# Kernel optimization log

Measured on AMD Instinct MI355X. Metric: run time of the kernel, lower is better.

## Reference

```python
import jax, jax.numpy as jnp
import numpy as np

B, N, L, K, C1 = 128, 300, 600, 19, 100  # batch, num_cnns, input_length, filter_size, fc hidden
PS = 7  # pool size == stride
LC = L - (K - 1)               # 582, conv output length
LP = (LC - PS) // PS + 1       # 83, pooled length
NC = 2                         # num_classes
EPS = 1e-5


def _bn(x, g, b, m, v):
    # eval-mode batchnorm, params broadcast along given axes already
    return g * (x - m) * jax.lax.rsqrt(v + EPS) + b


def setup_inputs() -> dict:
    key = jax.random.key(0)
    ks = jax.random.split(key, 20)
    f = lambda i, shape, s=0.1: (jax.random.normal(ks[i], shape, dtype=jnp.float32) * s)
    pv = lambda i, shape: (jax.random.uniform(ks[i], shape, dtype=jnp.float32) + 0.5)
    return {
        'x': jax.random.normal(ks[0], (B, 4, L), dtype=jnp.float32),
        'conv_w': f(1, (N, 4, K)), 'conv_b': f(2, (N,)),
        'bn1_g': pv(3, (N,)), 'bn1_b': f(4, (N,)), 'bn1_m': f(5, (N,)), 'bn1_v': pv(6, (N,)),
        'fc1_w': f(7, (N, C1, LP)), 'fc1_b': f(8, (N, C1)),
        'bn2_g': pv(9, (N, C1)), 'bn2_b': f(10, (N, C1)), 'bn2_m': f(11, (N, C1)), 'bn2_v': pv(12, (N, C1)),
        'fc2_w': f(13, (N, C1)), 'fc2_b': f(14, (N,)),
        'bn3_g': pv(15, (N,)), 'bn3_b': f(16, (N,)), 'bn3_m': f(17, (N,)), 'bn3_v': pv(18, (N,)),
        'final_w': f(19, (NC, N)), 'final_b': jnp.zeros((NC,), dtype=jnp.float32),
    }


def reference(x, conv_w, conv_b, bn1_g, bn1_b, bn1_m, bn1_v,
              fc1_w, fc1_b, bn2_g, bn2_b, bn2_m, bn2_v,
              fc2_w, fc2_b, bn3_g, bn3_b, bn3_m, bn3_v,
              final_w, final_b):
    # grouped conv on a repeated input == plain conv with 4 in-channels, N out-channels
    h = jax.lax.conv_general_dilated(x, conv_w, window_strides=(1,), padding='VALID',
                                     dimension_numbers=('NCH', 'OIH', 'NCH'))  # [B,N,582]
    h = h + conv_b[None, :, None]
    h = _bn(h, bn1_g[None, :, None], bn1_b[None, :, None], bn1_m[None, :, None], bn1_v[None, :, None])
    h = jnp.exp(h)
    # MaxPool1d(7,7): [B,N,582] -> [B,N,83]
    h = jax.lax.reduce_window(h, -jnp.inf, jax.lax.max,
                              window_dimensions=(1, 1, PS), window_strides=(1, 1, PS), padding='VALID')
    # grouped 1x1 conv == per-unit dense: [B,N,83] x [N,100,83] -> [B,N,100]
    h = jnp.einsum('bnp,nhp->bnh', h, fc1_w) + fc1_b[None]
    h = jax.nn.relu(_bn(h, bn2_g[None], bn2_b[None], bn2_m[None], bn2_v[None]))
    # second grouped 1x1 conv: [B,N,100] x [N,100] -> [B,N]
    h = jnp.einsum('bnh,nh->bn', h, fc2_w) + fc2_b[None]
    h = jax.nn.relu(_bn(h, bn3_g[None], bn3_b[None], bn3_m[None], bn3_v[None]))
    return h @ final_w.T + final_b  # [B,num_classes]
```

## Files before the change

### kernel.cpp

```cpp
#include <hip/hip_runtime.h>
#include <math.h>

#define EPS_ 1e-5f

__global__ __launch_bounds__(256) void kP(const float* __restrict__ conv_w,
                                          float* __restrict__ cw4) {
    const int cq = blockIdx.x;
    const int c  = cq / 5;
    const int kq = cq - c * 5;
    for (int n = threadIdx.x; n < 300; n += 256) {
        float4 v;
        const int k0 = 4 * kq;
        v.x = (k0 + 0 < 19) ? conv_w[n * 76 + c * 19 + k0 + 0] : 0.f;
        v.y = (k0 + 1 < 19) ? conv_w[n * 76 + c * 19 + k0 + 1] : 0.f;
        v.z = (k0 + 2 < 19) ? conv_w[n * 76 + c * 19 + k0 + 2] : 0.f;
        v.w = (k0 + 3 < 19) ? conv_w[n * 76 + c * 19 + k0 + 3] : 0.f;
        reinterpret_cast<float4*>(cw4)[(c * 5 + kq) * 300 + n] = v;
    }
}

__global__ __launch_bounds__(64) void kA(
        const float* __restrict__ x,
        const float* __restrict__ cw4,
        const float* __restrict__ conv_b,
        const float* __restrict__ g1, const float* __restrict__ b1,
        const float* __restrict__ m1, const float* __restrict__ v1,
        float* __restrict__ pooled)
{
    const int id  = blockIdx.x;
    const int b   = id / 112;
    const int sub = id - b * 112;
    if (sub >= 105) return;
    const int ng  = sub / 21;
    const int pc  = sub - ng * 21;
    const int p0c = pc * 4;
    const int p0  = (p0c > 79) ? 79 : p0c;
    const int lane = threadIdx.x;
    const int n   = ng * 64 + lane;
    const int nc  = (n < 300) ? n : 299;

    const float4* w4 = reinterpret_cast<const float4*>(cw4);

    float acc[28];
    #pragma unroll
    for (int i = 0; i < 28; ++i) acc[i] = 0.f;

    #pragma unroll 1
    for (int c = 0; c < 4; ++c) {
        const float* xc = x + b * 2400 + c * 600 + 7 * p0;
        float xw[46];
        #pragma unroll
        for (int j = 0; j < 46; ++j) xw[j] = xc[j];
        #pragma unroll
        for (int kq = 0; kq < 5; ++kq) {
            const float4 wv = w4[(c * 5 + kq) * 300 + nc];
            const int ni = (kq == 4) ? 3 : 4;
            #pragma unroll
            for (int i = 0; i < ni; ++i) {
                const int k = 4 * kq + i;
                const float wvv = (i == 0) ? wv.x : (i == 1) ? wv.y
                                : (i == 2) ? wv.z : wv.w;
                #pragma unroll
                for (int p = 0; p < 4; ++p)
                    #pragma unroll
                    for (int q = 0; q < 7; ++q)
                        acc[p * 7 + q] = fmaf(xw[7 * p + q + k], wvv,
                                              acc[p * 7 + q]);
            }
        }
    }

    const float A1 = g1[nc] * rsqrtf(v1[nc] + EPS_);
    const float B1 = fmaf(A1, conv_b[nc] - m1[nc], b1[nc]);
    if (n < 300) {
        float* op = pooled + ((size_t)n * 83 + p0) * 128 + b;
        #pragma unroll
        for (int p = 0; p < 4; ++p) {
            float mx = -INFINITY;
            #pragma unroll
            for (int q = 0; q < 7; ++q)
                mx = fmaxf(mx, fmaf(A1, acc[p * 7 + q], B1));
            op[p * 128] = __expf(mx);
        }
    }
}

__global__ __launch_bounds__(256, 2) void kB(
        const float* __restrict__ pooled,
        const float* __restrict__ fc1w,
        const float* __restrict__ fc1b,
        const float* __restrict__ g2, const float* __restrict__ b2,
        const float* __restrict__ m2, const float* __restrict__ v2,
        const float* __restrict__ fc2w,
        const float* __restrict__ fc2b,
        const float* __restrict__ g3, const float* __restrict__ b3,
        const float* __restrict__ m3, const float* __restrict__ v3,
        float* __restrict__ sout)
{
    __shared__ __align__(16) float sW[83 * 116];
    __shared__ float sRed[4][64];
    const int id  = blockIdx.x;
    const int n   = id >> 1;
    const int bh  = id & 1;
    const int tid = threadIdx.x;

    {
        const float* src = fc1w + (size_t)n * 8300;
        for (int i = tid; i < 8300; i += 256) {
            const int h = i / 83, p = i - h * 83;
            sW[p * 116 + h] = src[i];
        }
        for (int i = tid; i < 83 * 16; i += 256) {
            const int p = i / 16, h = 100 + (i - p * 16);
            sW[p * 116 + h] = 0.f;
        }
    }
    __syncthreads();

    const int lane = tid & 63;
    const int wv   = __builtin_amdgcn_readfirstlane(tid >> 6);
    const int h0   = wv * 28;
    const int bb   = bh * 64 + lane;

    const float* pp = pooled + (size_t)n * 83 * 128 + bb;

    float acc[28];
    #pragma unroll
    for (int j = 0; j < 28; ++j) acc[j] = 0.f;

    #pragma unroll 4
    for (int p = 0; p < 83; ++p) {
        const float pv = pp[p * 128];
        const float* wrow = sW + p * 116 + h0;
        #pragma unroll
        for (int jq = 0; jq < 7; ++jq) {
            const float4 w = *reinterpret_cast<const float4*>(wrow + 4 * jq);
            acc[jq * 4 + 0] = fmaf(w.x, pv, acc[jq * 4 + 0]);
            acc[jq * 4 + 1] = fmaf(w.y, pv, acc[jq * 4 + 1]);
            acc[jq * 4 + 2] = fmaf(w.z, pv, acc[jq * 4 + 2]);
            acc[jq * 4 + 3] = fmaf(w.w, pv, acc[jq * 4 + 3]);
        }
    }

    const int nh = (wv < 3) ? 28 : 16;
    float part = 0.f;
    for (int j = 0; j < nh; ++j) {
        const int hi = n * 100 + h0 + j;
        const float A2 = g2[hi] * rsqrtf(v2[hi] + EPS_);
        const float C2 = fmaf(A2, fc1b[hi] - m2[hi], b2[hi]);
        part = fmaf(fmaxf(fmaf(A2, acc[j], C2), 0.f), fc2w[hi], part);
    }
    sRed[wv][lane] = part;
    __syncthreads();

    if (tid < 64) {
        float s = sRed[0][tid] + sRed[1][tid] + sRed[2][tid] + sRed[3][tid];
        s += fc2b[n];
        const float A3 = g3[n] * rsqrtf(v3[n] + EPS_);
        const float z = fmaf(A3, s - m3[n], b3[n]);
        sout[n * 128 + bh * 64 + tid] = fmaxf(z, 0.f);
    }
}

__global__ __launch_bounds__(64) void kC(
        const float* __restrict__ sout,
        const float* __restrict__ fw,
        const float* __restrict__ fb,
        float* __restrict__ out)
{
    const int b = blockIdx.x, t = threadIdx.x;
    float a0 = 0.f, a1 = 0.f;
    for (int nn = t; nn < 300; nn += 64) {
        const float v = sout[nn * 128 + b];
        a0 = fmaf(v, fw[nn], a0);
        a1 = fmaf(v, fw[300 + nn], a1);
    }
    #pragma unroll
    for (int off = 32; off > 0; off >>= 1) {
        a0 += __shfl_xor(a0, off, 64);
        a1 += __shfl_xor(a1, off, 64);
    }
    if (t == 0) {
        out[b * 2 + 0] = a0 + fb[0];
        out[b * 2 + 1] = a1 + fb[1];
    }
}

extern "C" void kernel_launch(void* const* d_in, const int* in_sizes, int n_in,
                              void* d_out, int out_size, void* d_ws, size_t ws_size,
                              hipStream_t stream) {
    const float* x      = (const float*)d_in[0];
    const float* conv_w = (const float*)d_in[1];
    const float* conv_b = (const float*)d_in[2];
    const float* g1 = (const float*)d_in[3];
    const float* b1 = (const float*)d_in[4];
    const float* m1 = (const float*)d_in[5];
    const float* v1 = (const float*)d_in[6];
    const float* fc1_w = (const float*)d_in[7];
    const float* fc1_b = (const float*)d_in[8];
    const float* g2 = (const float*)d_in[9];
    const float* b2 = (const float*)d_in[10];
    const float* m2 = (const float*)d_in[11];
    const float* v2 = (const float*)d_in[12];
    const float* fc2_w = (const float*)d_in[13];
    const float* fc2_b = (const float*)d_in[14];
    const float* g3 = (const float*)d_in[15];
    const float* b3 = (const float*)d_in[16];
    const float* m3 = (const float*)d_in[17];
    const float* v3 = (const float*)d_in[18];
    const float* fw = (const float*)d_in[19];
    const float* fb = (const float*)d_in[20];
    float* out = (float*)d_out;

    float* pooled = (float*)d_ws;
    float* cw4    = pooled + (size_t)300 * 83 * 128;
    float* sout   = cw4 + 24000;

    kP<<<20, 256, 0, stream>>>(conv_w, cw4);
    kA<<<128 * 112, 64, 0, stream>>>(x, cw4, conv_b, g1, b1, m1, v1, pooled);
    kB<<<600, 256, 0, stream>>>(pooled, fc1_w, fc1_b, g2, b2, m2, v2,
                                fc2_w, fc2_b, g3, b3, m3, v3, sout);
    kC<<<128, 64, 0, stream>>>(sout, fw, fb, out);
}
```

Measured before the change: 174.3 us.

## Compute conv stage with fp16 MFMA matrix instructions instead of scalar FMAs

```diff
diff --git a/kernel.cpp b/kernel.cpp
--- a/kernel.cpp
+++ b/kernel.cpp
@@ -3,85 +3,114 @@
 
 #define EPS_ 1e-5f
 
-__global__ __launch_bounds__(256) void kP(const float* __restrict__ conv_w,
-                                          float* __restrict__ cw4) {
-    const int cq = blockIdx.x;
-    const int c  = cq / 5;
-    const int kq = cq - c * 5;
-    for (int n = threadIdx.x; n < 300; n += 256) {
-        float4 v;
-        const int k0 = 4 * kq;
-        v.x = (k0 + 0 < 19) ? conv_w[n * 76 + c * 19 + k0 + 0] : 0.f;
-        v.y = (k0 + 1 < 19) ? conv_w[n * 76 + c * 19 + k0 + 1] : 0.f;
-        v.z = (k0 + 2 < 19) ? conv_w[n * 76 + c * 19 + k0 + 2] : 0.f;
-        v.w = (k0 + 3 < 19) ? conv_w[n * 76 + c * 19 + k0 + 3] : 0.f;
-        reinterpret_cast<float4*>(cw4)[(c * 5 + kq) * 300 + n] = v;
-    }
-}
-
-__global__ __launch_bounds__(64) void kA(
+typedef _Float16 half8 __attribute__((ext_vector_type(8)));
+typedef float floatx4 __attribute__((ext_vector_type(4)));
+
+__global__ __launch_bounds__(256) void kW(const float* __restrict__ conv_w,
+                                          unsigned short* __restrict__ wT) {
+    const int idx = blockIdx.x * 256 + threadIdx.x;
+    if (idx >= 304 * 96) return;
+    const int n = idx / 96, k = idx - n * 96;
+    const int c = k / 24, kk = k - c * 24;
+    float v = (n < 300 && kk < 19) ? conv_w[n * 76 + c * 19 + kk] : 0.f;
+    union { _Float16 h; unsigned short u; } cv;
+    cv.h = (_Float16)v;
+    wT[idx] = cv.u;
+}
+
+__global__ __launch_bounds__(64) void kM(
         const float* __restrict__ x,
-        const float* __restrict__ cw4,
+        const unsigned short* __restrict__ wT,
         const float* __restrict__ conv_b,
         const float* __restrict__ g1, const float* __restrict__ b1,
         const float* __restrict__ m1, const float* __restrict__ v1,
         float* __restrict__ pooled)
 {
-    const int id  = blockIdx.x;
-    const int b   = id / 112;
-    const int sub = id - b * 112;
-    if (sub >= 105) return;
-    const int ng  = sub / 21;
-    const int pc  = sub - ng * 21;
-    const int p0c = pc * 4;
-    const int p0  = (p0c > 79) ? 79 : p0c;
+    const int id = blockIdx.x;
+    const int b  = id / 24;
+    const int nt = id - b * 24;
+    if (nt >= 19) return;
     const int lane = threadIdx.x;
-    const int n   = ng * 64 + lane;
-    const int nc  = (n < 300) ? n : 299;
-
-    const float4* w4 = reinterpret_cast<const float4*>(cw4);
-
-    float acc[28];
-    #pragma unroll
-    for (int i = 0; i < 28; ++i) acc[i] = 0.f;
-
-    #pragma unroll 1
-    for (int c = 0; c < 4; ++c) {
-        const float* xc = x + b * 2400 + c * 600 + 7 * p0;
-        float xw[46];
+    const int ln   = lane & 15;
+    const int quad = lane >> 4;
+    const int n0   = nt * 16;
+
+    __shared__ float xs[4 * 704];
+    __shared__ float dbuf[16 * 116];
+
+    for (int i = lane; i < 4 * 704; i += 64) {
+        const int c = i / 704, t = i - c * 704;
+        xs[i] = (t < 600) ? x[b * 2400 + c * 600 + t] : 0.f;
+    }
+
+    half8 bf[3];
+    {
+        const unsigned short* wrow = wT + (n0 + ln) * 96 + quad * 8;
         #pragma unroll
-        for (int j = 0; j < 46; ++j) xw[j] = xc[j];
-        #pragma unroll
-        for (int kq = 0; kq < 5; ++kq) {
-            const float4 wv = w4[(c * 5 + kq) * 300 + nc];
-            const int ni = (kq == 4) ? 3 : 4;
+        for (int s = 0; s < 3; ++s) {
+            union { int4 i; half8 h; } u;
+            u.i = *reinterpret_cast<const int4*>(wrow + 32 * s);
+            bf[s] = u.h;
+        }
+    }
+
+    int cS[3], oS[3];
+    #pragma unroll
+    for (int s = 0; s < 3; ++s) {
+        const int kg0 = 32 * s + 8 * quad;
+        cS[s] = kg0 / 24; oS[s] = kg0 - cS[s] * 24;
+    }
+
+    const int nq = lane & 3;
+    float A1w[4], B1w[4];
+    #pragma unroll
+    for (int w = 0; w < 4; ++w) {
+        const int n = n0 + 4 * nq + w;
+        const int nc = (n < 300) ? n : 299;
+        A1w[w] = g1[nc] * rsqrtf(v1[nc] + EPS_);
+        B1w[w] = fmaf(A1w[w], conv_b[nc] - m1[nc], b1[nc]);
+    }
+    __syncthreads();
+
+    for (int ci = 0; ci < 6; ++ci) {
+        const int t0 = 112 * ci;
+        #pragma unroll 1
+        for (int mt = 0; mt < 7; ++mt) {
+            const int tb = t0 + 16 * mt + ln;
+            floatx4 acc = {0.f, 0.f, 0.f, 0.f};
             #pragma unroll
-            for (int i = 0; i < ni; ++i) {
-                const int k = 4 * kq + i;
-                const float wvv = (i == 0) ? wv.x : (i == 1) ? wv.y
-                                : (i == 2) ? wv.z : wv.w;
+            for (int s = 0; s < 3; ++s) {
+                const float* px = &xs[cS[s] * 704 + tb + oS[s]];
+                half8 af;
                 #pragma unroll
-                for (int p = 0; p < 4; ++p)
+                for (int j = 0; j < 8; ++j)
+                    af[j] = (_Float16)px[j];
+                acc = __builtin_amdgcn_mfma_f32_16x16x32_f16(af, bf[s], acc,
+                                                             0, 0, 0);
+            }
+            float* dp = &dbuf[ln * 116 + 16 * mt + quad * 4];
+            float4 dv = make_float4(acc[0], acc[1], acc[2], acc[3]);
+            *reinterpret_cast<float4*>(dp) = dv;
+        }
+        __syncthreads();
+        const int pl = lane >> 2;
+        const int npool = (ci < 5) ? 16 : 3;
+        if (pl < npool) {
+            const int pg = 16 * ci + pl;
+            #pragma unroll
+            for (int w = 0; w < 4; ++w) {
+                const int n = n0 + 4 * nq + w;
+                if (n < 300) {
+                    const float* dq = &dbuf[(4 * nq + w) * 116 + 7 * pl];
+                    float mx = -INFINITY;
                     #pragma unroll
                     for (int q = 0; q < 7; ++q)
-                        acc[p * 7 + q] = fmaf(xw[7 * p + q + k], wvv,
-                                              acc[p * 7 + q]);
+                        mx = fmaxf(mx, fmaf(A1w[w], dq[q], B1w[w]));
+                    pooled[((size_t)n * 83 + pg) * 128 + b] = __expf(mx);
+                }
             }
         }
-    }
-
-    const float A1 = g1[nc] * rsqrtf(v1[nc] + EPS_);
-    const float B1 = fmaf(A1, conv_b[nc] - m1[nc], b1[nc]);
-    if (n < 300) {
-        float* op = pooled + ((size_t)n * 83 + p0) * 128 + b;
-        #pragma unroll
-        for (int p = 0; p < 4; ++p) {
-            float mx = -INFINITY;
-            #pragma unroll
-            for (int q = 0; q < 7; ++q)
-                mx = fmaxf(mx, fmaf(A1, acc[p * 7 + q], B1));
-            op[p * 128] = __expf(mx);
-        }
+        __syncthreads();
     }
 }
 
@@ -213,11 +242,11 @@
     float* out = (float*)d_out;
 
     float* pooled = (float*)d_ws;
-    float* cw4    = pooled + (size_t)300 * 83 * 128;
-    float* sout   = cw4 + 24000;
-
-    kP<<<20, 256, 0, stream>>>(conv_w, cw4);
-    kA<<<128 * 112, 64, 0, stream>>>(x, cw4, conv_b, g1, b1, m1, v1, pooled);
+    float* sout   = pooled + (size_t)300 * 83 * 128;
+    unsigned short* wT = (unsigned short*)(sout + 38400);
+
+    kW<<<114, 256, 0, stream>>>(conv_w, wT);
+    kM<<<128 * 24, 64, 0, stream>>>(x, wT, conv_b, g1, b1, m1, v1, pooled);
     kB<<<600, 256, 0, stream>>>(pooled, fc1_w, fc1_b, g2, b2, m2, v2,
                                 fc2_w, fc2_b, g3, b3, m3, v3, sout);
     kC<<<128, 64, 0, stream>>>(sout, fw, fb, out);
```

Result: slower. 186.9 us (+7.3%).

## Split fc1 hidden dimension across two blocks and defer bn3 to final kernel

Applied to the files above, without the earlier changes.

```diff
diff --git a/kernel.cpp b/kernel.cpp
--- a/kernel.cpp
+++ b/kernel.cpp
@@ -85,85 +85,80 @@
     }
 }
 
-__global__ __launch_bounds__(256, 2) void kB(
+__global__ __launch_bounds__(256) void kB(
         const float* __restrict__ pooled,
         const float* __restrict__ fc1w,
         const float* __restrict__ fc1b,
         const float* __restrict__ g2, const float* __restrict__ b2,
         const float* __restrict__ m2, const float* __restrict__ v2,
         const float* __restrict__ fc2w,
+        float* __restrict__ sp)
+{
+    __shared__ float sW[83 * 60];
+    __shared__ float sRed[4][64];
+    const int id  = blockIdx.x;
+    const int n   = id >> 2;
+    const int rem = id & 3;
+    const int bh  = rem >> 1;
+    const int hq  = rem & 1;
+    const int tid = threadIdx.x;
+
+    {
+        const float* src = fc1w + (size_t)n * 8300 + hq * 50 * 83;
+        for (int i = tid; i < 4150; i += 256) {
+            const int h = i / 83, p = i - h * 83;
+            sW[p * 60 + h] = src[i];
+        }
+        for (int i = tid; i < 830; i += 256) {
+            const int p = i / 10, h = 50 + (i - p * 10);
+            sW[p * 60 + h] = 0.f;
+        }
+    }
+    __syncthreads();
+
+    const int lane = tid & 63;
+    const int wv   = __builtin_amdgcn_readfirstlane(tid >> 6);
+    const int h0   = wv * 13;
+    const int nh   = (wv < 3) ? 13 : 11;
+    const int bb   = bh * 64 + lane;
+
+    const float* pp = pooled + (size_t)n * 83 * 128 + bb;
+
+    float acc[13];
+    #pragma unroll
+    for (int j = 0; j < 13; ++j) acc[j] = 0.f;
+
+    #pragma unroll 4
+    for (int p = 0; p < 83; ++p) {
+        const float pv = pp[p * 128];
+        const float* wrow = sW + p * 60 + h0;
+        #pragma unroll
+        for (int j = 0; j < 13; ++j)
+            acc[j] = fmaf(wrow[j], pv, acc[j]);
+    }
+
+    const int hbase = n * 100 + hq * 50 + h0;
+    float part = 0.f;
+    for (int j = 0; j < nh; ++j) {
+        const int hi = hbase + j;
+        const float A2 = g2[hi] * rsqrtf(v2[hi] + EPS_);
+        const float C2 = fmaf(A2, fc1b[hi] - m2[hi], b2[hi]);
+        part = fmaf(fmaxf(fmaf(A2, acc[j], C2), 0.f), fc2w[hi], part);
+    }
+    sRed[wv][lane] = part;
+    __syncthreads();
+
+    if (tid < 64) {
+        const float s = sRed[0][tid] + sRed[1][tid] + sRed[2][tid] + sRed[3][tid];
+        sp[((size_t)hq * 300 + n) * 128 + bh * 64 + tid] = s;
+    }
+}
+
+__global__ __launch_bounds__(64) void kC(
+        const float* __restrict__ sp,
         const float* __restrict__ fc2b,
         const float* __restrict__ g3, const float* __restrict__ b3,
         const float* __restrict__ m3, const float* __restrict__ v3,
-        float* __restrict__ sout)
-{
-    __shared__ __align__(16) float sW[83 * 116];
-    __shared__ float sRed[4][64];
-    const int id  = blockIdx.x;
-    const int n   = id >> 1;
-    const int bh  = id & 1;
-    const int tid = threadIdx.x;
-
-    {
-        const float* src = fc1w + (size_t)n * 8300;
-        for (int i = tid; i < 8300; i += 256) {
-            const int h = i / 83, p = i - h * 83;
-            sW[p * 116 + h] = src[i];
-        }
-        for (int i = tid; i < 83 * 16; i += 256) {
-            const int p = i / 16, h = 100 + (i - p * 16);
-            sW[p * 116 + h] = 0.f;
-        }
-    }
-    __syncthreads();
-
-    const int lane = tid & 63;
-    const int wv   = __builtin_amdgcn_readfirstlane(tid >> 6);
-    const int h0   = wv * 28;
-    const int bb   = bh * 64 + lane;
-
-    const float* pp = pooled + (size_t)n * 83 * 128 + bb;
-
-    float acc[28];
-    #pragma unroll
-    for (int j = 0; j < 28; ++j) acc[j] = 0.f;
-
-    #pragma unroll 4
-    for (int p = 0; p < 83; ++p) {
-        const float pv = pp[p * 128];
-        const float* wrow = sW + p * 116 + h0;
-        #pragma unroll
-        for (int jq = 0; jq < 7; ++jq) {
-            const float4 w = *reinterpret_cast<const float4*>(wrow + 4 * jq);
-            acc[jq * 4 + 0] = fmaf(w.x, pv, acc[jq * 4 + 0]);
-            acc[jq * 4 + 1] = fmaf(w.y, pv, acc[jq * 4 + 1]);
-            acc[jq * 4 + 2] = fmaf(w.z, pv, acc[jq * 4 + 2]);
-            acc[jq * 4 + 3] = fmaf(w.w, pv, acc[jq * 4 + 3]);
-        }
-    }
-
-    const int nh = (wv < 3) ? 28 : 16;
-    float part = 0.f;
-    for (int j = 0; j < nh; ++j) {
-        const int hi = n * 100 + h0 + j;
-        const float A2 = g2[hi] * rsqrtf(v2[hi] + EPS_);
-        const float C2 = fmaf(A2, fc1b[hi] - m2[hi], b2[hi]);
-        part = fmaf(fmaxf(fmaf(A2, acc[j], C2), 0.f), fc2w[hi], part);
-    }
-    sRed[wv][lane] = part;
-    __syncthreads();
-
-    if (tid < 64) {
-        float s = sRed[0][tid] + sRed[1][tid] + sRed[2][tid] + sRed[3][tid];
-        s += fc2b[n];
-        const float A3 = g3[n] * rsqrtf(v3[n] + EPS_);
-        const float z = fmaf(A3, s - m3[n], b3[n]);
-        sout[n * 128 + bh * 64 + tid] = fmaxf(z, 0.f);
-    }
-}
-
-__global__ __launch_bounds__(64) void kC(
-        const float* __restrict__ sout,
         const float* __restrict__ fw,
         const float* __restrict__ fb,
         float* __restrict__ out)
@@ -171,9 +166,11 @@
     const int b = blockIdx.x, t = threadIdx.x;
     float a0 = 0.f, a1 = 0.f;
     for (int nn = t; nn < 300; nn += 64) {
-        const float v = sout[nn * 128 + b];
-        a0 = fmaf(v, fw[nn], a0);
-        a1 = fmaf(v, fw[300 + nn], a1);
+        const float s = sp[nn * 128 + b] + sp[(300 + nn) * 128 + b] + fc2b[nn];
+        const float A3 = g3[nn] * rsqrtf(v3[nn] + EPS_);
+        const float z = fmaxf(fmaf(A3, s - m3[nn], b3[nn]), 0.f);
+        a0 = fmaf(z, fw[nn], a0);
+        a1 = fmaf(z, fw[300 + nn], a1);
     }
     #pragma unroll
     for (int off = 32; off > 0; off >>= 1) {
@@ -213,12 +210,12 @@
     float* out = (float*)d_out;
 
     float* pooled = (float*)d_ws;
-    float* cw4    = pooled + (size_t)300 * 83 * 128;
-    float* sout   = cw4 + 24000;
+    float* sp     = pooled + (size_t)300 * 83 * 128;
+    float* cw4    = sp + 76800;
 
     kP<<<20, 256, 0, stream>>>(conv_w, cw4);
     kA<<<128 * 112, 64, 0, stream>>>(x, cw4, conv_b, g1, b1, m1, v1, pooled);
-    kB<<<600, 256, 0, stream>>>(pooled, fc1_w, fc1_b, g2, b2, m2, v2,
-                                fc2_w, fc2_b, g3, b3, m3, v3, sout);
-    kC<<<128, 64, 0, stream>>>(sout, fw, fb, out);
-}
+    kB<<<1200, 256, 0, stream>>>(pooled, fc1_w, fc1_b, g2, b2, m2, v2,
+                                 fc2_w, sp);
+    kC<<<128, 64, 0, stream>>>(sp, fc2_b, g3, b3, m3, v3, fw, fb, out);
+}
```

Result: no change. 173.3 us (median of 2 runs) (-0.6%).
